# Optimization experiments

Hardware: AMD Instinct MI355X
Metric: run time of the kernel (lower is better)

The kernel has to match this reference:

```python
import jax, jax.numpy as jnp
import numpy as np

TEMPERATURE = 0.07


def setup_inputs() -> dict:
    B, NB_PER, K, M, D = 32, 128, 8, 4, 256  # batches, bsl1k per batch, dict targets per batch, embeds per target, feat dim
    key = jax.random.key(0)
    kb, kd = jax.random.split(key)
    feats_bsl1k = jax.random.normal(kb, (B * NB_PER, D), dtype=jnp.float32)
    feats_dict = jax.random.normal(kd, (B * K * M, D), dtype=jnp.float32)
    # dict side: per batch, K distinct targets (first one is the mouthing word), M embeddings each
    batch_dict = np.repeat(np.arange(B), K * M).astype(np.int32)
    targets_dict = np.repeat(np.arange(B * K), M).astype(np.int32)  # sorted, distinct across batches
    one_mouth = np.concatenate([np.ones(1, np.int32), np.zeros(K - 1, np.int32)])
    is_mouthing_dict = np.tile(np.repeat(one_mouth, M), B).astype(np.int32)
    # bsl1k side: half the clips carry the batch's mouthing target, half are background (-1)
    batch_bsl1k = np.repeat(np.arange(B), NB_PER).astype(np.int32)
    tb = np.full((B, NB_PER), -1, dtype=np.int32)
    tb[:, : NB_PER // 2] = (np.arange(B, dtype=np.int32) * K)[:, None]
    targets_bsl1k = tb.reshape(-1)
    unique_targets = np.arange(B * K, dtype=np.int32)  # == unique_consecutive(targets_dict)
    return {
        "feats_bsl1k": feats_bsl1k,
        "feats_dict": feats_dict,
        "targets_bsl1k": jnp.asarray(targets_bsl1k),
        "targets_dict": jnp.asarray(targets_dict),
        "batch_bsl1k": jnp.asarray(batch_bsl1k),
        "batch_dict": jnp.asarray(batch_dict),
        "is_mouthing_dict": jnp.asarray(is_mouthing_dict),
        "unique_targets": jnp.asarray(unique_targets),
        "n_batches": B,
    }


def _loss(feats_bsl1k, feats_dict, targets_bsl1k, targets_dict, batch_bsl1k,
          batch_dict, is_mouthing_dict, unique_targets, n_batches):
    G = unique_targets.shape[0]
    fb = feats_bsl1k / jnp.linalg.norm(feats_bsl1k, axis=1, keepdims=True)
    fd = feats_dict / jnp.linalg.norm(feats_dict, axis=1, keepdims=True)
    dist = (fb @ fd.T) / TEMPERATURE  # [Nb, Nd]

    # group index of each dict embedding (unique_targets is sorted)
    g_idx = jnp.searchsorted(unique_targets, targets_dict).astype(jnp.int32)  # [Nd]
    # per-batch mouthing word (exactly one per batch, mirrors .item() in torch)
    mouth_word = jax.ops.segment_max(
        jnp.where(is_mouthing_dict == 1, targets_dict, -1), batch_dict, num_segments=n_batches)
    group_batch = jax.ops.segment_max(batch_dict, g_idx, num_segments=G)
    group_is_mouth = jax.ops.segment_max(is_mouthing_dict, g_idx, num_segments=G)

    # match[i, g]: bsl1k embedding i matches dict target group g (== match_multi collapsed per target)
    is_fg = targets_bsl1k != -1
    mw = mouth_word[batch_bsl1k]  # [Nb]
    match = jnp.where(
        is_fg[:, None],
        unique_targets[None, :] == mw[:, None],
        (group_batch[None, :] == batch_bsl1k[:, None]) & (group_is_mouth[None, :] == 0),
    )  # [Nb, G] bool

    # diff_batch_match: matched pairs from different batches are excluded from the denominator
    DB = match[:, g_idx] & (batch_bsl1k[:, None] != batch_dict[None, :])  # [Nb, Nd]

    c = jax.lax.stop_gradient(jnp.max(dist))  # shared lse shift; cancels in den - num
    E = jnp.exp(dist - c)                     # raw pair weights (numerator)
    A = jnp.where(DB, 0.0, E)                 # denominator weights with cross-batch matches removed
    matchf = match.astype(dist.dtype)

    Ecg = jax.ops.segment_sum(E.T, g_idx, num_segments=G)  # [G, Nb] column-group sums
    Acg = jax.ops.segment_sum(A.T, g_idx, num_segments=G)  # [G, Nb]

    # numerator[g] = lse over cross product {matched bsl1k rows} x {group-g dict cols}
    num_sum = jnp.einsum('gi,ig->g', Ecg, matchf)
    # denominator[g] = lse over union (group cols OR matched rows) minus cross-batch matches,
    # via inclusion-exclusion: cols + rows - intersection
    t1 = jax.ops.segment_sum(A.sum(0), g_idx, num_segments=G)
    t2 = jnp.einsum('ig,i->g', matchf, A.sum(1))
    t3 = jnp.einsum('gi,ig->g', Acg, matchf)
    den_sum = t1 + t2 - t3
    return jnp.mean(jnp.log(den_sum) - jnp.log(num_sum))


def reference(feats_bsl1k, feats_dict, targets_bsl1k, targets_dict, batch_bsl1k,
              batch_dict, is_mouthing_dict, unique_targets, n_batches):
    return _loss(feats_bsl1k, feats_dict, targets_bsl1k, targets_dict, batch_bsl1k,
                 batch_dict, is_mouthing_dict, unique_targets, n_batches)
```

## Files before the change

kernel.cpp:

```cpp
#include <hip/hip_runtime.h>
#include <math.h>

#define INVT (1.0f / 0.07f)
#define CSHIFT (1.0f / 0.07f)

using bf16x8 = __attribute__((ext_vector_type(8))) short;
using f32x4  = __attribute__((ext_vector_type(4))) float;

__device__ __forceinline__ int lower_bound_i(const int* a, int n, int v) {
    int lo = 0, hi = n;
    while (lo < hi) { int mid = (lo + hi) >> 1; if (a[mid] < v) lo = mid + 1; else hi = mid; }
    return lo;
}

__device__ __forceinline__ unsigned short f2bf(float x) {
    unsigned int u = __float_as_uint(x);
    unsigned int r = (u + 0x7fffu + ((u >> 16) & 1u)) >> 16;
    return (unsigned short)r;
}

__device__ __forceinline__ float agent_ld(const float* p) {
    return __hip_atomic_load(p, __ATOMIC_RELAXED, __HIP_MEMORY_SCOPE_AGENT);
}

__global__ void k_prep(const float* __restrict__ fb, const float* __restrict__ fd,
                       int Nb, int Nd, int D,
                       unsigned short* __restrict__ fbt, unsigned short* __restrict__ fdt,
                       float* __restrict__ rowpart, float* __restrict__ colpart,
                       unsigned int* __restrict__ dcnt,
                       const int* __restrict__ td, const int* __restrict__ bd,
                       const int* __restrict__ im,
                       int* __restrict__ mouth_word) {
    int zidx = blockIdx.x * blockDim.x + threadIdx.x;
    int z1 = 4 * Nb, z2 = z1 + 24 * Nd, z3 = z2 + 1025;
    if (zidx < z1) rowpart[zidx] = 0.f;
    else if (zidx < z2) colpart[zidx - z1] = 0.f;
    else if (zidx < z3) dcnt[zidx - z2] = 0u;

    int gw = zidx >> 6;
    int lane = threadIdx.x & 63;
    int ktiles = D >> 5;
    if (gw < Nb + Nd) {
        const float* row; unsigned short* ob; int rt, r;
        if (gw < Nb) {
            row = fb + (size_t)gw * D; ob = fbt; rt = gw >> 4; r = gw & 15;
        } else {
            int j = gw - Nb;
            row = fd + (size_t)j * D; ob = fdt; rt = j >> 4; r = j & 15;
        }
        float s = 0.f;
        for (int d = lane * 4; d < D; d += 256) {
            float4 v = *(const float4*)(row + d);
            s += v.x * v.x + v.y * v.y + v.z * v.z + v.w * v.w;
        }
        #pragma unroll
        for (int m = 32; m >= 1; m >>= 1) s += __shfl_xor(s, m, 64);
        float inv = rsqrtf(s);
        for (int d = lane * 4; d < D; d += 256) {
            float4 v = *(const float4*)(row + d);
            ushort4 o;
            o.x = f2bf(v.x * inv); o.y = f2bf(v.y * inv);
            o.z = f2bf(v.z * inv); o.w = f2bf(v.w * inv);
            int kt = d >> 5, kk = d & 31;
            int slot = (kk >> 3) * 16 + r, elem = kk & 7;
            *(ushort4*)(ob + (((size_t)(rt * ktiles + kt)) << 9) + slot * 8 + elem) = o;
        }
    }
    if (blockIdx.x == 0) {
        int t = threadIdx.x;
        for (int i = t; i < Nb; i += blockDim.x) mouth_word[i] = -1;
        __syncthreads();
        for (int j = t; j < Nd; j += blockDim.x) {
            if (im[j] == 1) atomicMax(&mouth_word[bd[j]], td[j]);
        }
    }
}

__global__ __launch_bounds__(256, 4)
void k_main(const unsigned short* __restrict__ fbt, const unsigned short* __restrict__ fdt,
            const int* __restrict__ tb, const int* __restrict__ bb_arr,
            const int* __restrict__ td, const int* __restrict__ bd,
            const int* __restrict__ im, const int* __restrict__ ut,
            const int* __restrict__ mouth_word,
            int Nb, int Nd, int D, int G,
            float* __restrict__ rowpart, float* __restrict__ colpart,
            unsigned int* __restrict__ dcnt, float* __restrict__ out) {
    __shared__ float cnum[64], ct1[64], ct3[64], rsum[64];
    __shared__ int lastflag;

    int t = threadIdx.x, lane = t & 63, wid = t >> 6;
    int wr = wid >> 1, wc = wid & 1;
    int bm = blockIdx.x * 64, bn = blockIdx.y * 64;
    int l15 = lane & 15, lhi = lane >> 4;

    if (t < 64) { cnum[t] = 0.f; ct1[t] = 0.f; ct3[t] = 0.f; rsum[t] = 0.f; }

    int ktiles = D >> 5;
    const unsigned short* a0p = fbt + (((size_t)(((bm >> 4) + wr * 2) * ktiles)) << 9) + lane * 8;
    const unsigned short* a1p = a0p + ((size_t)ktiles << 9);
    const unsigned short* b0p = fdt + (((size_t)(((bn >> 4) + wc * 2) * ktiles)) << 9) + lane * 8;
    const unsigned short* b1p = b0p + ((size_t)ktiles << 9);

    f32x4 acc[2][2] = {};
    #pragma unroll 8
    for (int kt = 0; kt < ktiles; ++kt) {
        size_t o = (size_t)kt << 9;
        bf16x8 a0 = *(const bf16x8*)(a0p + o);
        bf16x8 a1 = *(const bf16x8*)(a1p + o);
        bf16x8 b0 = *(const bf16x8*)(b0p + o);
        bf16x8 b1 = *(const bf16x8*)(b1p + o);
        acc[0][0] = __builtin_amdgcn_mfma_f32_16x16x32_bf16(a0, b0, acc[0][0], 0, 0, 0);
        acc[0][1] = __builtin_amdgcn_mfma_f32_16x16x32_bf16(a0, b1, acc[0][1], 0, 0, 0);
        acc[1][0] = __builtin_amdgcn_mfma_f32_16x16x32_bf16(a1, b0, acc[1][0], 0, 0, 0);
        acc[1][1] = __builtin_amdgcn_mfma_f32_16x16x32_bf16(a1, b1, acc[1][1], 0, 0, 0);
    }

    int cgb[2], cgm[2], cgc[2];
    #pragma unroll
    for (int nj = 0; nj < 2; ++nj) {
        int col = bn + wc * 32 + nj * 16 + l15;
        cgb[nj] = bd[col]; cgm[nj] = im[col]; cgc[nj] = td[col];
    }

    float pnum[2] = {0.f, 0.f}, pt1[2] = {0.f, 0.f}, pt3[2] = {0.f, 0.f};
    float prow[2][4];

    #pragma unroll
    for (int mi = 0; mi < 2; ++mi) {
        #pragma unroll
        for (int r = 0; r < 4; ++r) {
            int i = bm + wr * 32 + mi * 16 + lhi * 4 + r;
            int tbi = tb[i], bbi = bb_arr[i];
            int mw = mouth_word[bbi];
            bool fg = (tbi != -1);
            float pr = 0.f;
            #pragma unroll
            for (int nj = 0; nj < 2; ++nj) {
                float e = __expf(acc[mi][nj][r] * INVT - CSHIFT);
                bool match = fg ? (cgc[nj] == mw) : ((cgb[nj] == bbi) && (cgm[nj] == 0));
                float a = (match && (bbi != cgb[nj])) ? 0.f : e;
                pnum[nj] += match ? e : 0.f;
                pt1[nj] += a;
                pt3[nj] += match ? a : 0.f;
                pr += a;
            }
            prow[mi][r] = pr;
        }
    }

    __syncthreads();

    #pragma unroll
    for (int nj = 0; nj < 2; ++nj) {
        float n = pnum[nj], x1 = pt1[nj], x3 = pt3[nj];
        n  += __shfl_xor(n, 16, 64);  n  += __shfl_xor(n, 32, 64);
        x1 += __shfl_xor(x1, 16, 64); x1 += __shfl_xor(x1, 32, 64);
        x3 += __shfl_xor(x3, 16, 64); x3 += __shfl_xor(x3, 32, 64);
        if (lhi == 0) {
            int c = wc * 32 + nj * 16 + l15;
            atomicAdd(&cnum[c], n); atomicAdd(&ct1[c], x1); atomicAdd(&ct3[c], x3);
        }
    }
    #pragma unroll
    for (int mi = 0; mi < 2; ++mi) {
        #pragma unroll
        for (int r = 0; r < 4; ++r) {
            float v = prow[mi][r];
            v += __shfl_xor(v, 1, 64); v += __shfl_xor(v, 2, 64);
            v += __shfl_xor(v, 4, 64); v += __shfl_xor(v, 8, 64);
            if (l15 == 0) atomicAdd(&rsum[wr * 32 + mi * 16 + lhi * 4 + r], v);
        }
    }
    __syncthreads();

    float* cp = colpart + (size_t)(blockIdx.x & 7) * 3 * Nd;
    if (t < 64) {
        atomicAdd(&cp[bn + t], cnum[t]);
        atomicAdd(&cp[Nd + bn + t], ct1[t]);
        atomicAdd(&cp[2 * Nd + bn + t], ct3[t]);
    } else if (t < 128) {
        atomicAdd(&rowpart[(size_t)(blockIdx.y & 3) * Nb + bm + (t - 64)], rsum[t - 64]);
    }

    asm volatile("s_waitcnt vmcnt(0)" ::: "memory");
    __syncthreads();
    if (t == 0) {
        int lf = 0;
        unsigned int old = atomicAdd(&dcnt[blockIdx.x * 16], 1u);
        if (old == gridDim.y - 1) {
            unsigned int old2 = atomicAdd(&dcnt[1024], 1u);
            lf = (old2 == gridDim.x - 1) ? 1 : 0;
        }
        lastflag = lf;
    }
    __syncthreads();
    if (!lastflag) return;

    __shared__ float t2g[1024], bgs[1024], red[256];
    for (int i = t; i < 1024; i += 256) { t2g[i] = 0.f; bgs[i] = 0.f; }
    __syncthreads();
    for (int i = t; i < Nb; i += 256) {
        float r = agent_ld(&rowpart[i]) + agent_ld(&rowpart[Nb + i])
                + agent_ld(&rowpart[2 * Nb + i]) + agent_ld(&rowpart[3 * Nb + i]);
        int tbi = tb[i], bbi = bb_arr[i] & 1023;
        if (tbi != -1) {
            int g = lower_bound_i(ut, G, mouth_word[bbi]);
            atomicAdd(&t2g[g & 1023], r);
        } else {
            atomicAdd(&bgs[bbi], r);
        }
    }
    __syncthreads();
    float acc2 = 0.f;
    for (int g = t; g < G; g += 256) {
        int s = lower_bound_i(td, Nd, ut[g]);
        int e = (g + 1 < G) ? lower_bound_i(td, Nd, ut[g + 1]) : Nd;
        float sn = 0.f, s1 = 0.f, s3 = 0.f;
        for (int c = s; c < e; ++c) {
            #pragma unroll
            for (int p = 0; p < 8; ++p) {
                const float* base = colpart + (size_t)p * 3 * Nd;
                sn += agent_ld(&base[c]);
                s1 += agent_ld(&base[Nd + c]);
                s3 += agent_ld(&base[2 * Nd + c]);
            }
        }
        int gb = bd[s], gm = im[s];
        float t2 = t2g[g & 1023];
        if (gm == 0 && gb >= 0 && gb < 1024) t2 += bgs[gb];
        acc2 += logf(s1 + t2 - s3) - logf(sn);
    }
    red[t] = acc2;
    __syncthreads();
    for (int k = 128; k >= 1; k >>= 1) {
        if (t < k) red[t] += red[t + k];
        __syncthreads();
    }
    if (t == 0) out[0] = red[0] / (float)G;
}

extern "C" void kernel_launch(void* const* d_in, const int* in_sizes, int n_in,
                              void* d_out, int out_size, void* d_ws, size_t ws_size,
                              hipStream_t stream) {
    const float* fb = (const float*)d_in[0];
    const float* fd = (const float*)d_in[1];
    const int* tb = (const int*)d_in[2];
    const int* td = (const int*)d_in[3];
    const int* bb = (const int*)d_in[4];
    const int* bd = (const int*)d_in[5];
    const int* im = (const int*)d_in[6];
    const int* ut = (const int*)d_in[7];

    int Nb = in_sizes[2];
    int Nd = in_sizes[3];
    int G  = in_sizes[7];
    int D  = in_sizes[0] / Nb;
    float* out = (float*)d_out;

    char* p = (char*)d_ws;
    unsigned short* fbt = (unsigned short*)p; p += (size_t)Nb * D * sizeof(unsigned short);
    unsigned short* fdt = (unsigned short*)p; p += (size_t)Nd * D * sizeof(unsigned short);
    float* rowpart = (float*)p; p += (size_t)4 * Nb * sizeof(float);
    float* colpart = (float*)p; p += (size_t)24 * Nd * sizeof(float);
    int* mouth_word = (int*)p;  p += (size_t)Nb * sizeof(int);
    unsigned int* dcnt = (unsigned int*)p; p += 1025 * sizeof(unsigned int);

    {
        int waves = Nb + Nd;
        int blocks = (waves + 3) / 4;
        k_prep<<<blocks, 256, 0, stream>>>(fb, fd, Nb, Nd, D, fbt, fdt,
                                           rowpart, colpart, dcnt,
                                           td, bd, im, mouth_word);
    }

    dim3 grid(Nb / 64, Nd / 64);
    k_main<<<grid, 256, 0, stream>>>(fbt, fdt, tb, bb, td, bd, im, ut, mouth_word,
                                     Nb, Nd, D, G,
                                     rowpart, colpart, dcnt, out);
}
```

Before: 54.19 us.

## Distribute final reductions across row/column finisher blocks and prefetch MFMA operands

The tail reduction no longer runs in one last block. Per-row-tile and per-column-tile completion counters let the block that finishes a row tile or column tile fold its partial sums into global t2g/bgs and merged column arrays. Only a small per-group log reduction is left for the final block. The GEMM loop also software-prefetches the next k-tile operands ahead of the MFMAs, at the cost of more global atomics and counters to zero.

```diff
diff --git a/kernel.cpp b/kernel.cpp
--- a/kernel.cpp
+++ b/kernel.cpp
@@ -22,20 +22,19 @@
 __device__ __forceinline__ float agent_ld(const float* p) {
     return __hip_atomic_load(p, __ATOMIC_RELAXED, __HIP_MEMORY_SCOPE_AGENT);
 }
+__device__ __forceinline__ void agent_st(float* p, float v) {
+    __hip_atomic_store(p, v, __ATOMIC_RELAXED, __HIP_MEMORY_SCOPE_AGENT);
+}
 
 __global__ void k_prep(const float* __restrict__ fb, const float* __restrict__ fd,
                        int Nb, int Nd, int D,
                        unsigned short* __restrict__ fbt, unsigned short* __restrict__ fdt,
-                       float* __restrict__ rowpart, float* __restrict__ colpart,
-                       unsigned int* __restrict__ dcnt,
+                       unsigned int* __restrict__ zbase, int zcount,
                        const int* __restrict__ td, const int* __restrict__ bd,
                        const int* __restrict__ im,
                        int* __restrict__ mouth_word) {
     int zidx = blockIdx.x * blockDim.x + threadIdx.x;
-    int z1 = 4 * Nb, z2 = z1 + 24 * Nd, z3 = z2 + 1025;
-    if (zidx < z1) rowpart[zidx] = 0.f;
-    else if (zidx < z2) colpart[zidx - z1] = 0.f;
-    else if (zidx < z3) dcnt[zidx - z2] = 0u;
+    if (zidx < zcount) zbase[zidx] = 0u;
 
     int gw = zidx >> 6;
     int lane = threadIdx.x & 63;
@@ -84,9 +83,12 @@
             const int* __restrict__ mouth_word,
             int Nb, int Nd, int D, int G,
             float* __restrict__ rowpart, float* __restrict__ colpart,
+            float* __restrict__ mnum, float* __restrict__ m1, float* __restrict__ m3,
+            float* __restrict__ t2g, float* __restrict__ bgs,
+            unsigned int* __restrict__ rowcnt, unsigned int* __restrict__ colcnt,
             unsigned int* __restrict__ dcnt, float* __restrict__ out) {
     __shared__ float cnum[64], ct1[64], ct3[64], rsum[64];
-    __shared__ int lastflag;
+    __shared__ int rowflag, colflag, lastflag;
 
     int t = threadIdx.x, lane = t & 63, wid = t >> 6;
     int wr = wid >> 1, wc = wid & 1;
@@ -102,18 +104,28 @@
     const unsigned short* b1p = b0p + ((size_t)ktiles << 9);
 
     f32x4 acc[2][2] = {};
-    #pragma unroll 8
-    for (int kt = 0; kt < ktiles; ++kt) {
-        size_t o = (size_t)kt << 9;
-        bf16x8 a0 = *(const bf16x8*)(a0p + o);
-        bf16x8 a1 = *(const bf16x8*)(a1p + o);
-        bf16x8 b0 = *(const bf16x8*)(b0p + o);
-        bf16x8 b1 = *(const bf16x8*)(b1p + o);
-        acc[0][0] = __builtin_amdgcn_mfma_f32_16x16x32_bf16(a0, b0, acc[0][0], 0, 0, 0);
-        acc[0][1] = __builtin_amdgcn_mfma_f32_16x16x32_bf16(a0, b1, acc[0][1], 0, 0, 0);
-        acc[1][0] = __builtin_amdgcn_mfma_f32_16x16x32_bf16(a1, b0, acc[1][0], 0, 0, 0);
-        acc[1][1] = __builtin_amdgcn_mfma_f32_16x16x32_bf16(a1, b1, acc[1][1], 0, 0, 0);
-    }
+    bf16x8 ca0 = *(const bf16x8*)a0p;
+    bf16x8 ca1 = *(const bf16x8*)a1p;
+    bf16x8 cb0 = *(const bf16x8*)b0p;
+    bf16x8 cb1 = *(const bf16x8*)b1p;
+    size_t o = 0;
+    #pragma unroll 7
+    for (int kt = 0; kt + 1 < ktiles; ++kt) {
+        o += 512;
+        bf16x8 na0 = *(const bf16x8*)(a0p + o);
+        bf16x8 na1 = *(const bf16x8*)(a1p + o);
+        bf16x8 nb0 = *(const bf16x8*)(b0p + o);
+        bf16x8 nb1 = *(const bf16x8*)(b1p + o);
+        acc[0][0] = __builtin_amdgcn_mfma_f32_16x16x32_bf16(ca0, cb0, acc[0][0], 0, 0, 0);
+        acc[0][1] = __builtin_amdgcn_mfma_f32_16x16x32_bf16(ca0, cb1, acc[0][1], 0, 0, 0);
+        acc[1][0] = __builtin_amdgcn_mfma_f32_16x16x32_bf16(ca1, cb0, acc[1][0], 0, 0, 0);
+        acc[1][1] = __builtin_amdgcn_mfma_f32_16x16x32_bf16(ca1, cb1, acc[1][1], 0, 0, 0);
+        ca0 = na0; ca1 = na1; cb0 = nb0; cb1 = nb1;
+    }
+    acc[0][0] = __builtin_amdgcn_mfma_f32_16x16x32_bf16(ca0, cb0, acc[0][0], 0, 0, 0);
+    acc[0][1] = __builtin_amdgcn_mfma_f32_16x16x32_bf16(ca0, cb1, acc[0][1], 0, 0, 0);
+    acc[1][0] = __builtin_amdgcn_mfma_f32_16x16x32_bf16(ca1, cb0, acc[1][0], 0, 0, 0);
+    acc[1][1] = __builtin_amdgcn_mfma_f32_16x16x32_bf16(ca1, cb1, acc[1][1], 0, 0, 0);
 
     int cgb[2], cgm[2], cgc[2];
     #pragma unroll
@@ -185,49 +197,59 @@
     asm volatile("s_waitcnt vmcnt(0)" ::: "memory");
     __syncthreads();
     if (t == 0) {
-        int lf = 0;
-        unsigned int old = atomicAdd(&dcnt[blockIdx.x * 16], 1u);
-        if (old == gridDim.y - 1) {
-            unsigned int old2 = atomicAdd(&dcnt[1024], 1u);
-            lf = (old2 == gridDim.x - 1) ? 1 : 0;
-        }
-        lastflag = lf;
-    }
-    __syncthreads();
-    if (!lastflag) return;
-
-    __shared__ float t2g[1024], bgs[1024], red[256];
-    for (int i = t; i < 1024; i += 256) { t2g[i] = 0.f; bgs[i] = 0.f; }
-    __syncthreads();
-    for (int i = t; i < Nb; i += 256) {
+        rowflag = (atomicAdd(&rowcnt[blockIdx.x * 16], 1u) == gridDim.y - 1) ? 1 : 0;
+        colflag = (atomicAdd(&colcnt[blockIdx.y * 16], 1u) == gridDim.x - 1) ? 1 : 0;
+    }
+    __syncthreads();
+    int nfin = rowflag + colflag;
+    if (nfin == 0) return;
+
+    if (rowflag && t < 64) {
+        int i = bm + t;
         float r = agent_ld(&rowpart[i]) + agent_ld(&rowpart[Nb + i])
                 + agent_ld(&rowpart[2 * Nb + i]) + agent_ld(&rowpart[3 * Nb + i]);
         int tbi = tb[i], bbi = bb_arr[i] & 1023;
         if (tbi != -1) {
             int g = lower_bound_i(ut, G, mouth_word[bbi]);
-            atomicAdd(&t2g[g & 1023], r);
+            atomicAdd(&t2g[g], r);
         } else {
             atomicAdd(&bgs[bbi], r);
         }
     }
-    __syncthreads();
+    if (colflag && t < 192) {
+        int c = t / 3, arr = t - c * 3;
+        int col = bn + c;
+        float s0 = 0.f;
+        #pragma unroll
+        for (int p = 0; p < 8; ++p)
+            s0 += agent_ld(&colpart[(size_t)p * 3 * Nd + (size_t)arr * Nd + col]);
+        float* dst = (arr == 0 ? mnum : (arr == 1 ? m1 : m3)) + col;
+        agent_st(dst, s0);
+    }
+
+    asm volatile("s_waitcnt vmcnt(0)" ::: "memory");
+    __syncthreads();
+    if (t == 0) {
+        unsigned int newv = atomicAdd(dcnt, (unsigned int)nfin) + (unsigned int)nfin;
+        lastflag = (newv == gridDim.x + gridDim.y) ? 1 : 0;
+    }
+    __syncthreads();
+    if (!lastflag) return;
+
+    __shared__ float red[256];
     float acc2 = 0.f;
     for (int g = t; g < G; g += 256) {
         int s = lower_bound_i(td, Nd, ut[g]);
         int e = (g + 1 < G) ? lower_bound_i(td, Nd, ut[g + 1]) : Nd;
         float sn = 0.f, s1 = 0.f, s3 = 0.f;
         for (int c = s; c < e; ++c) {
-            #pragma unroll
-            for (int p = 0; p < 8; ++p) {
-                const float* base = colpart + (size_t)p * 3 * Nd;
-                sn += agent_ld(&base[c]);
-                s1 += agent_ld(&base[Nd + c]);
-                s3 += agent_ld(&base[2 * Nd + c]);
-            }
+            sn += agent_ld(&mnum[c]);
+            s1 += agent_ld(&m1[c]);
+            s3 += agent_ld(&m3[c]);
         }
         int gb = bd[s], gm = im[s];
-        float t2 = t2g[g & 1023];
-        if (gm == 0 && gb >= 0 && gb < 1024) t2 += bgs[gb];
+        float t2 = agent_ld(&t2g[g]);
+        if (gm == 0 && gb >= 0 && gb < 1024) t2 += agent_ld(&bgs[gb]);
         acc2 += logf(s1 + t2 - s3) - logf(sn);
     }
     red[t] = acc2;
@@ -260,21 +282,31 @@
     char* p = (char*)d_ws;
     unsigned short* fbt = (unsigned short*)p; p += (size_t)Nb * D * sizeof(unsigned short);
     unsigned short* fdt = (unsigned short*)p; p += (size_t)Nd * D * sizeof(unsigned short);
-    float* rowpart = (float*)p; p += (size_t)4 * Nb * sizeof(float);
-    float* colpart = (float*)p; p += (size_t)24 * Nd * sizeof(float);
-    int* mouth_word = (int*)p;  p += (size_t)Nb * sizeof(int);
-    unsigned int* dcnt = (unsigned int*)p; p += 1025 * sizeof(unsigned int);
+    char* zstart = p;
+    float* rowpart = (float*)p;  p += (size_t)4 * Nb * sizeof(float);
+    float* colpart = (float*)p;  p += (size_t)24 * Nd * sizeof(float);
+    float* t2g = (float*)p;      p += 1024 * sizeof(float);
+    float* bgs = (float*)p;      p += 1024 * sizeof(float);
+    unsigned int* rowcnt = (unsigned int*)p; p += 64 * 16 * sizeof(unsigned int);
+    unsigned int* colcnt = (unsigned int*)p; p += 16 * 16 * sizeof(unsigned int);
+    unsigned int* dcnt = (unsigned int*)p;   p += 16 * sizeof(unsigned int);
+    int zcount = (int)((p - zstart) / 4);
+    float* mnum = (float*)p; p += (size_t)Nd * sizeof(float);
+    float* m1 = (float*)p;   p += (size_t)Nd * sizeof(float);
+    float* m3 = (float*)p;   p += (size_t)Nd * sizeof(float);
+    int* mouth_word = (int*)p; p += (size_t)Nb * sizeof(int);
 
     {
         int waves = Nb + Nd;
         int blocks = (waves + 3) / 4;
         k_prep<<<blocks, 256, 0, stream>>>(fb, fd, Nb, Nd, D, fbt, fdt,
-                                           rowpart, colpart, dcnt,
+                                           (unsigned int*)zstart, zcount,
                                            td, bd, im, mouth_word);
     }
 
     dim3 grid(Nb / 64, Nd / 64);
     k_main<<<grid, 256, 0, stream>>>(fbt, fdt, tb, bb, td, bd, im, ut, mouth_word,
                                      Nb, Nd, D, G,
-                                     rowpart, colpart, dcnt, out);
-}
+                                     rowpart, colpart, mnum, m1, m3, t2g, bgs,
+                                     rowcnt, colcnt, dcnt, out);
+}
```

New measurement: 44.94 us. 17.1% less time.
